# Performance work log

Hardware: AMD Instinct MI355X
Metric: run time of the kernel (lower is better)

Reference implementation:

```python
import jax, jax.numpy as jnp
import numpy as np

D_IN = 1024
D_OUT = 1024
SEQ = 2048
BATCH = 4


def setup_inputs() -> dict:
    key = jax.random.key(0)
    k_x, k_q, k_k, k_v = jax.random.split(key, 4)
    scale = 1.0 / np.sqrt(D_IN)  # ~ torch Linear init scale
    x = jax.random.normal(k_x, (BATCH, SEQ, D_IN), dtype=jnp.float32)
    # torch nn.Linear weights have shape [d_out, d_in]; y = x @ W.T
    Wq = jax.random.uniform(k_q, (D_OUT, D_IN), jnp.float32, -scale, scale)
    Wk = jax.random.uniform(k_k, (D_OUT, D_IN), jnp.float32, -scale, scale)
    Wv = jax.random.uniform(k_v, (D_OUT, D_IN), jnp.float32, -scale, scale)
    return {"x": x, "Wq": Wq, "Wk": Wk, "Wv": Wv}


def reference(x, Wq, Wk, Wv):
    # projections (no bias, qkv_bias=False)
    q = jnp.einsum("bsd,ed->bse", x, Wq)  # [B,S,D_OUT]
    k = jnp.einsum("bsd,ed->bse", x, Wk)
    v = jnp.einsum("bsd,ed->bse", x, Wv)
    scores = jnp.einsum("bqe,bke->bqk", q, k)  # [B,S,S]
    seq = scores.shape[-1]
    causal = jnp.tril(jnp.ones((seq, seq), dtype=bool))  # keep lower-tri
    scores = jnp.where(causal[None], scores, -jnp.inf)
    # note: original scales AFTER masking: softmax(scores / sqrt(d_k))
    inv_sqrt_dk = 1.0 / np.sqrt(k.shape[-1]).astype(np.float32)
    weights = jax.nn.softmax(scores * inv_sqrt_dk, axis=-1)
    # dropout p=0.0 (eval-equivalent): identity
    return jnp.einsum("bqk,bke->bqe", weights, v)
```

## Files before the change

kernel.cpp:

```cpp
#include <hip/hip_runtime.h>
#include <hip/hip_bf16.h>

typedef __bf16 v8bf __attribute__((ext_vector_type(8)));
typedef float v4f __attribute__((ext_vector_type(4)));

#define GBL_AS(p) ((const __attribute__((address_space(1))) unsigned int*)(p))
#define LDS_AS(p) ((__attribute__((address_space(3))) unsigned int*)(p))

#define WAIT_VM4() __builtin_amdgcn_s_waitcnt(0x0F74)
#define WAIT_VM6() __builtin_amdgcn_s_waitcnt(0x0F76)
#define WAIT_VM0() __builtin_amdgcn_s_waitcnt(0x0F70)

__global__ void cast_f32_bf16(const float* __restrict__ src,
                              __hip_bfloat16* __restrict__ dst, int n) {
  int i = (blockIdx.x * 256 + threadIdx.x) * 4;
  if (i >= n) return;
  float4 f = *(const float4*)(src + i);
  union { __hip_bfloat16 h[4]; uint2 u; } pk;
  pk.h[0] = __float2bfloat16(f.x);
  pk.h[1] = __float2bfloat16(f.y);
  pk.h[2] = __float2bfloat16(f.z);
  pk.h[3] = __float2bfloat16(f.w);
  *(uint2*)(dst + i) = pk.u;
}

__global__ void cast_w3(const float* __restrict__ a, const float* __restrict__ b,
                        const float* __restrict__ c, __hip_bfloat16* __restrict__ dst) {
  int seg = blockIdx.x >> 10;
  const float* src = seg == 0 ? a : (seg == 1 ? b : c);
  int i = ((blockIdx.x & 1023) * 256 + threadIdx.x) * 4;
  float4 f = *(const float4*)(src + i);
  union { __hip_bfloat16 h[4]; uint2 u; } pk;
  pk.h[0] = __float2bfloat16(f.x);
  pk.h[1] = __float2bfloat16(f.y);
  pk.h[2] = __float2bfloat16(f.z);
  pk.h[3] = __float2bfloat16(f.w);
  *(uint2*)(dst + seg * 1048576 + i) = pk.u;
}

__global__ __launch_bounds__(256, 2)
void gemm_proj(const __hip_bfloat16* __restrict__ A, int lda,
               const __hip_bfloat16* __restrict__ B, long sBb, int ldb,
               __hip_bfloat16* __restrict__ C, long sCb, int ldc,
               float scale, __hip_bfloat16* __restrict__ vTp) {
  const int tid = threadIdx.x;
  const int l = tid & 63, w = tid >> 6;
  const int z  = blockIdx.x >> 3;
  const int nb = (blockIdx.x & 7) << 7;
  const int mb = blockIdx.y << 8;

  B += (long)z * sBb;

  __shared__ alignas(16) __hip_bfloat16 As[3][256 * 32];
  __shared__ alignas(16) __hip_bfloat16 Bs[3][128 * 32];

  v4f acc[8][4] = {};
  const int wm = (w >> 1) << 7;
  const int wn = (w & 1) << 6;

  const int qa0 = 0 * 256 + w * 64 + l, ra0 = qa0 >> 2;
  const int qa1 = 1 * 256 + w * 64 + l, ra1 = qa1 >> 2;
  const int qa2 = 2 * 256 + w * 64 + l, ra2 = qa2 >> 2;
  const int qa3 = 3 * 256 + w * 64 + l, ra3 = qa3 >> 2;
  const __hip_bfloat16* sA0 = A + (long)(mb + ra0) * lda + (((qa0 & 3) ^ ((ra0 >> 1) & 3)) << 3);
  const __hip_bfloat16* sA1 = A + (long)(mb + ra1) * lda + (((qa1 & 3) ^ ((ra1 >> 1) & 3)) << 3);
  const __hip_bfloat16* sA2 = A + (long)(mb + ra2) * lda + (((qa2 & 3) ^ ((ra2 >> 1) & 3)) << 3);
  const __hip_bfloat16* sA3 = A + (long)(mb + ra3) * lda + (((qa3 & 3) ^ ((ra3 >> 1) & 3)) << 3);
  const int qb0 = 0 * 256 + w * 64 + l, rb0 = qb0 >> 2;
  const int qb1 = 1 * 256 + w * 64 + l, rb1 = qb1 >> 2;
  const __hip_bfloat16* sB0 = B + (long)(nb + rb0) * ldb + (((qb0 & 3) ^ ((rb0 >> 1) & 3)) << 3);
  const __hip_bfloat16* sB1 = B + (long)(nb + rb1) * ldb + (((qb1 & 3) ^ ((rb1 >> 1) & 3)) << 3);

  const int arow = wm + (l & 15);
  const int ldsA = arow * 32 + ((((l >> 4) ^ ((arow >> 1) & 3))) << 3);
  const int brow = wn + (l & 15);
  const int ldsB = brow * 32 + ((((l >> 4) ^ ((brow >> 1) & 3))) << 3);

#define STAGE_P(K0, BUF) do {                                                   \
    __builtin_amdgcn_global_load_lds(GBL_AS(sA0 + (K0)),                        \
        LDS_AS(&As[BUF][0 * 2048 + w * 512]), 16, 0, 0);                        \
    __builtin_amdgcn_global_load_lds(GBL_AS(sA1 + (K0)),                        \
        LDS_AS(&As[BUF][1 * 2048 + w * 512]), 16, 0, 0);                        \
    __builtin_amdgcn_global_load_lds(GBL_AS(sA2 + (K0)),                        \
        LDS_AS(&As[BUF][2 * 2048 + w * 512]), 16, 0, 0);                        \
    __builtin_amdgcn_global_load_lds(GBL_AS(sA3 + (K0)),                        \
        LDS_AS(&As[BUF][3 * 2048 + w * 512]), 16, 0, 0);                        \
    __builtin_amdgcn_global_load_lds(GBL_AS(sB0 + (K0)),                        \
        LDS_AS(&Bs[BUF][0 * 2048 + w * 512]), 16, 0, 0);                        \
    __builtin_amdgcn_global_load_lds(GBL_AS(sB1 + (K0)),                        \
        LDS_AS(&Bs[BUF][1 * 2048 + w * 512]), 16, 0, 0);                        \
  } while (0)

#define COMPUTE_P(BI) do {                                                      \
    v8bf af[8], bfr[4];                                                         \
    _Pragma("unroll")                                                           \
    for (int i = 0; i < 8; ++i)                                                 \
      af[i]  = *(const v8bf*)(&As[BI][ldsA + i * 512]);                         \
    _Pragma("unroll")                                                           \
    for (int j = 0; j < 4; ++j)                                                 \
      bfr[j] = *(const v8bf*)(&Bs[BI][ldsB + j * 512]);                         \
    _Pragma("unroll")                                                           \
    for (int i = 0; i < 8; ++i)                                                 \
      _Pragma("unroll")                                                         \
      for (int j = 0; j < 4; ++j)                                               \
        acc[i][j] = __builtin_amdgcn_mfma_f32_16x16x32_bf16(af[i], bfr[j],      \
                                                            acc[i][j], 0, 0, 0);\
  } while (0)

#define KITER_P(IT) do {                                                        \
    if constexpr ((IT) < 31) WAIT_VM6(); else WAIT_VM0();                       \
    __builtin_amdgcn_s_barrier();                                               \
    if constexpr ((IT) < 30) STAGE_P((IT) * 32 + 64, ((IT) + 2) % 3);           \
    COMPUTE_P((IT) % 3);                                                        \
  } while (0)

  STAGE_P(0, 0);
  STAGE_P(32, 1);
  KITER_P(0);  KITER_P(1);  KITER_P(2);  KITER_P(3);  KITER_P(4);  KITER_P(5);
  KITER_P(6);  KITER_P(7);  KITER_P(8);  KITER_P(9);  KITER_P(10); KITER_P(11);
  KITER_P(12); KITER_P(13); KITER_P(14); KITER_P(15); KITER_P(16); KITER_P(17);
  KITER_P(18); KITER_P(19); KITER_P(20); KITER_P(21); KITER_P(22); KITER_P(23);
  KITER_P(24); KITER_P(25); KITER_P(26); KITER_P(27); KITER_P(28); KITER_P(29);
  KITER_P(30); KITER_P(31);
#undef KITER_P
#undef COMPUTE_P
#undef STAGE_P

  const int col0 = nb + wn + (l & 15);
  const int row0 = mb + wm + ((l >> 4) << 2);
  if (z < 2) {
    __hip_bfloat16* Cz = C + (long)z * sCb;
#pragma unroll
    for (int i = 0; i < 8; ++i)
#pragma unroll
      for (int r = 0; r < 4; ++r) {
        long ro = (long)(row0 + i * 16 + r) * ldc;
#pragma unroll
        for (int j = 0; j < 4; ++j)
          Cz[ro + col0 + j * 16] = __float2bfloat16(acc[i][j][r] * scale);
      }
  } else {
    const long b = row0 >> 11;
    const int seq0 = row0 & 2047;
#pragma unroll
    for (int i = 0; i < 8; ++i)
#pragma unroll
      for (int j = 0; j < 4; ++j) {
        union { __hip_bfloat16 h[4]; uint2 u; } pk;
#pragma unroll
        for (int r = 0; r < 4; ++r) pk.h[r] = __float2bfloat16(acc[i][j][r]);
        *(uint2*)(vTp + b * 2097152 + (long)(col0 + j * 16) * 2048 +
                  (seq0 + i * 16)) = pk.u;
      }
  }
}

__global__ __launch_bounds__(256, 3)
void gemm_score(const __hip_bfloat16* __restrict__ A, long sAb,
                const __hip_bfloat16* __restrict__ B, long sBb,
                __hip_bfloat16* __restrict__ C, long sCb,
                float scale, float* __restrict__ sums) {
  const int tid = threadIdx.x;
  const int l = tid & 63, w = tid >> 6;
  const int id = blockIdx.x;
  const int wk = (id & 7) * 68 + (id >> 3);
  const int z = wk / 136;
  const int t = wk - z * 136;
  int m = (int)((__builtin_sqrtf(8.0f * t + 1.0f) - 1.0f) * 0.5f);
  while ((m + 1) * (m + 2) / 2 <= t) ++m;
  while (m * (m + 1) / 2 > t) --m;
  const int mb = m << 7;
  const int nb = (t - m * (m + 1) / 2) << 7;

  const __hip_bfloat16* Az = A + (long)z * sAb;
  const __hip_bfloat16* Bz = B + (long)z * sBb;

  __shared__ alignas(16) __hip_bfloat16 As[3][128 * 32];
  __shared__ alignas(16) __hip_bfloat16 Bs[3][128 * 32];

  v4f acc[4][4] = {};
  const int wm = (w >> 1) * 64, wn = (w & 1) * 64;

  const int cb0 = w * 64;
  const int q0 = cb0 + l, r0s = q0 >> 2;
  const int c0s = ((q0 & 3) ^ ((r0s >> 1) & 3)) << 3;
  const int cb1 = 256 + w * 64;
  const int q1 = cb1 + l, r1s = q1 >> 2;
  const int c1s = ((q1 & 3) ^ ((r1s >> 1) & 3)) << 3;

  const __hip_bfloat16* Arow0 = Az + (long)(mb + r0s) * 1024 + c0s;
  const __hip_bfloat16* Arow1 = Az + (long)(mb + r1s) * 1024 + c1s;
  const __hip_bfloat16* Brow0 = Bz + (long)(nb + r0s) * 1024 + c0s;
  const __hip_bfloat16* Brow1 = Bz + (long)(nb + r1s) * 1024 + c1s;

  const int arow = wm + (l & 15);
  const int ldsA = arow * 32 + ((((l >> 4) ^ ((arow >> 1) & 3))) << 3);
  const int brow = wn + (l & 15);
  const int ldsB = brow * 32 + ((((l >> 4) ^ ((brow >> 1) & 3))) << 3);

#define STAGE_S(K0, BUF) do {                                                   \
    __builtin_amdgcn_global_load_lds(GBL_AS(Arow0 + (K0)),                      \
        LDS_AS(&As[BUF][cb0 * 8]), 16, 0, 0);                                   \
    __builtin_amdgcn_global_load_lds(GBL_AS(Brow0 + (K0)),                      \
        LDS_AS(&Bs[BUF][cb0 * 8]), 16, 0, 0);                                   \
    __builtin_amdgcn_global_load_lds(GBL_AS(Arow1 + (K0)),                      \
        LDS_AS(&As[BUF][cb1 * 8]), 16, 0, 0);                                   \
    __builtin_amdgcn_global_load_lds(GBL_AS(Brow1 + (K0)),                      \
        LDS_AS(&Bs[BUF][cb1 * 8]), 16, 0, 0);                                   \
  } while (0)

#define COMPUTE_S(BI) do {                                                      \
    v8bf af[4], bfr[4];                                                         \
    _Pragma("unroll")                                                           \
    for (int i = 0; i < 4; ++i) {                                               \
      af[i]  = *(const v8bf*)(&As[BI][ldsA + i * 512]);                         \
      bfr[i] = *(const v8bf*)(&Bs[BI][ldsB + i * 512]);                         \
    }                                                                           \
    _Pragma("unroll")                                                           \
    for (int i = 0; i < 4; ++i)                                                 \
      _Pragma("unroll")                                                         \
      for (int j = 0; j < 4; ++j)                                               \
        acc[i][j] = __builtin_amdgcn_mfma_f32_16x16x32_bf16(af[i], bfr[j],      \
                                                            acc[i][j], 0, 0, 0);\
  } while (0)

#define KITER_S(IT) do {                                                        \
    if constexpr ((IT) < 31) WAIT_VM4(); else WAIT_VM0();                       \
    __builtin_amdgcn_s_barrier();                                               \
    if constexpr ((IT) < 30) STAGE_S((IT) * 32 + 64, ((IT) + 2) % 3);           \
    COMPUTE_S((IT) % 3);                                                        \
  } while (0)

  STAGE_S(0, 0);
  STAGE_S(32, 1);
  KITER_S(0);  KITER_S(1);  KITER_S(2);  KITER_S(3);  KITER_S(4);  KITER_S(5);
  KITER_S(6);  KITER_S(7);  KITER_S(8);  KITER_S(9);  KITER_S(10); KITER_S(11);
  KITER_S(12); KITER_S(13); KITER_S(14); KITER_S(15); KITER_S(16); KITER_S(17);
  KITER_S(18); KITER_S(19); KITER_S(20); KITER_S(21); KITER_S(22); KITER_S(23);
  KITER_S(24); KITER_S(25); KITER_S(26); KITER_S(27); KITER_S(28); KITER_S(29);
  KITER_S(30); KITER_S(31);
#undef KITER_S
#undef COMPUTE_S
#undef STAGE_S

  __hip_bfloat16* Cz = C + (long)z * sCb;
  float* srow = sums + z * 2048;
  const int col0 = nb + wn + (l & 15);
  const int row0 = mb + wm + ((l >> 4) << 2);
#pragma unroll
  for (int i = 0; i < 4; ++i)
#pragma unroll
    for (int r = 0; r < 4; ++r) {
      const int mm = row0 + i * 16 + r;
      const long ro = (long)mm * 2048;
      float sp = 0.f;
#pragma unroll
      for (int j = 0; j < 4; ++j) {
        const int n = col0 + j * 16;
        float pv = (n <= mm) ? __expf(acc[i][j][r] * scale) : 0.0f;
        sp += pv;
        Cz[ro + n] = __float2bfloat16(pv);
      }
      sp += __shfl_xor(sp, 1);
      sp += __shfl_xor(sp, 2);
      sp += __shfl_xor(sp, 4);
      sp += __shfl_xor(sp, 8);
      if ((l & 15) == 0) atomicAdd(&srow[mm], sp);
    }
}

__global__ __launch_bounds__(256, 3)
void gemm_pv(const __hip_bfloat16* __restrict__ A, long sAb, int lda,
             const __hip_bfloat16* __restrict__ B, long sBb, int ldb,
             float* __restrict__ C, long sCb, int ldc,
             const float* __restrict__ sums) {
  const int tid = threadIdx.x;
  const int l = tid & 63, w = tid >> 6;
  const int id = blockIdx.x;
  const int x = id & 7, j = id >> 3;
  const int z = x >> 1;
  const int nb = (((x & 1) << 2) | (j & 3)) << 7;
  const int m = 15 - (j >> 2);
  const int mb = m << 7;
  const int kend = (m + 1) << 7;

  A += (long)z * sAb;
  B += (long)z * sBb;

  __shared__ alignas(16) __hip_bfloat16 As[3][128 * 32];
  __shared__ alignas(16) __hip_bfloat16 Bs[3][128 * 32];

  v4f acc[4][4] = {};
  const int wm = (w >> 1) * 64, wn = (w & 1) * 64;

  const int cb0 = w * 64;
  const int q0 = cb0 + l, r0s = q0 >> 2;
  const int c0s = ((q0 & 3) ^ ((r0s >> 1) & 3)) << 3;
  const int cb1 = 256 + w * 64;
  const int q1 = cb1 + l, r1s = q1 >> 2;
  const int c1s = ((q1 & 3) ^ ((r1s >> 1) & 3)) << 3;

  const __hip_bfloat16* Arow0 = A + (long)(mb + r0s) * lda + c0s;
  const __hip_bfloat16* Arow1 = A + (long)(mb + r1s) * lda + c1s;
  const __hip_bfloat16* Brow0 = B + (long)(nb + r0s) * ldb + c0s;
  const __hip_bfloat16* Brow1 = B + (long)(nb + r1s) * ldb + c1s;

  const int arow = wm + (l & 15);
  const int ldsA = arow * 32 + ((((l >> 4) ^ ((arow >> 1) & 3))) << 3);
  const int brow = wn + (l & 15);
  const int ldsB = brow * 32 + ((((l >> 4) ^ ((brow >> 1) & 3))) << 3);

  auto stage = [&](int k0, int buf) {
    __builtin_amdgcn_global_load_lds(GBL_AS(Arow0 + k0),
        LDS_AS(&As[buf][cb0 * 8]), 16, 0, 0);
    __builtin_amdgcn_global_load_lds(GBL_AS(Brow0 + k0),
        LDS_AS(&Bs[buf][cb0 * 8]), 16, 0, 0);
    __builtin_amdgcn_global_load_lds(GBL_AS(Arow1 + k0),
        LDS_AS(&As[buf][cb1 * 8]), 16, 0, 0);
    __builtin_amdgcn_global_load_lds(GBL_AS(Brow1 + k0),
        LDS_AS(&Bs[buf][cb1 * 8]), 16, 0, 0);
  };
  stage(0, 0);
  if (32 < kend) stage(32, 1);
  int bi = 0;
  for (int k0 = 0; k0 < kend; k0 += 32) {
    if (k0 + 32 < kend) WAIT_VM4(); else WAIT_VM0();
    __builtin_amdgcn_s_barrier();
    if (k0 + 64 < kend) stage(k0 + 64, bi == 0 ? 2 : bi - 1);
    v8bf af[4], bfr[4];
#pragma unroll
    for (int i = 0; i < 4; ++i) {
      af[i]  = *(const v8bf*)(&As[bi][ldsA + i * 512]);
      bfr[i] = *(const v8bf*)(&Bs[bi][ldsB + i * 512]);
    }
#pragma unroll
    for (int i = 0; i < 4; ++i)
#pragma unroll
      for (int jj = 0; jj < 4; ++jj)
        acc[i][jj] = __builtin_amdgcn_mfma_f32_16x16x32_bf16(af[i], bfr[jj], acc[i][jj], 0, 0, 0);
    bi = (bi == 2) ? 0 : bi + 1;
  }

  float* Cz = C + (long)z * sCb;
  const float* srow = sums + z * 2048;
  const int col0 = nb + wn + (l & 15);
  const int row0 = mb + wm + ((l >> 4) << 2);
#pragma unroll
  for (int i = 0; i < 4; ++i)
#pragma unroll
    for (int r = 0; r < 4; ++r) {
      const int mr = row0 + i * 16 + r;
      const float sc = 1.0f / srow[mr];
      const long ro = (long)mr * ldc;
#pragma unroll
      for (int jj = 0; jj < 4; ++jj)
        Cz[ro + col0 + jj * 16] = acc[i][jj][r] * sc;
    }
}

extern "C" void kernel_launch(void* const* d_in, const int* in_sizes, int n_in,
                              void* d_out, int out_size, void* d_ws, size_t ws_size,
                              hipStream_t stream) {
  const float* x  = (const float*)d_in[0];
  const float* Wq = (const float*)d_in[1];
  const float* Wk = (const float*)d_in[2];
  const float* Wv = (const float*)d_in[3];
  float* out = (float*)d_out;
  char* ws = (char*)d_ws;

  __hip_bfloat16* qkv = (__hip_bfloat16*)ws;
  __hip_bfloat16* vT  = (__hip_bfloat16*)(ws + 50331648);
  __hip_bfloat16* xb  = (__hip_bfloat16*)(ws + 67108864);
  __hip_bfloat16* Wb  = (__hip_bfloat16*)(ws + 83886080);
  __hip_bfloat16* P   = (__hip_bfloat16*)(ws + 67108864);
  float* sums         = (float*)(ws + 100663296);

  hipMemsetAsync(sums, 0, 8192 * sizeof(float), stream);

  cast_f32_bf16<<<8192, 256, 0, stream>>>(x, xb, 8388608);
  cast_w3<<<3072, 256, 0, stream>>>(Wq, Wk, Wv, Wb);

  gemm_proj<<<dim3(24, 32, 1), 256, 0, stream>>>(
      xb, 1024, Wb, 1048576L, 1024, qkv, 8388608L, 1024, 1.0f, vT);

  gemm_score<<<dim3(544, 1, 1), 256, 0, stream>>>(
      qkv, 2097152L, qkv + 8388608, 2097152L,
      P, 4194304L, 0.03125f, sums);

  gemm_pv<<<dim3(512, 1, 1), 256, 0, stream>>>(
      P, 4194304L, 2048, vT, 2097152L, 2048,
      out, 2097152L, 1024, sums);
}
```

Measured before the change: 230.8 us.

## Enlarge score and PV GEMM tiles to 256x128 with per-wave 128x64 outputs

Both the causal score GEMM and the P·V GEMM now use 256x128 block tiles, with each wave computing a 128x64 sub-tile (8x4 MFMA accumulators) instead of 128x128 tiles with 64x64 per wave. The score kernel's triangular tile enumeration is reworked for 256-row blocks, and both grids shrink (544→288 and 512→256 blocks), with launch bounds lowered to 2 blocks per CU. The aim is more MFMA work per LDS fragment load and less global traffic per FLOP. The cost is higher register and LDS use, lower occupancy, fewer blocks to spread over the CUs, and extra masked work on the diagonal.

```diff
diff --git a/kernel.cpp b/kernel.cpp
--- a/kernel.cpp
+++ b/kernel.cpp
@@ -7,7 +7,6 @@
 #define GBL_AS(p) ((const __attribute__((address_space(1))) unsigned int*)(p))
 #define LDS_AS(p) ((__attribute__((address_space(3))) unsigned int*)(p))
 
-#define WAIT_VM4() __builtin_amdgcn_s_waitcnt(0x0F74)
 #define WAIT_VM6() __builtin_amdgcn_s_waitcnt(0x0F76)
 #define WAIT_VM0() __builtin_amdgcn_s_waitcnt(0x0F70)
 
@@ -37,6 +36,7 @@
   pk.h[3] = __float2bfloat16(f.w);
   *(uint2*)(dst + seg * 1048576 + i) = pk.u;
 }
+
 
 __global__ __launch_bounds__(256, 2)
 void gemm_proj(const __hip_bfloat16* __restrict__ A, int lda,
@@ -155,7 +155,7 @@
   }
 }
 
-__global__ __launch_bounds__(256, 3)
+__global__ __launch_bounds__(256, 2)
 void gemm_score(const __hip_bfloat16* __restrict__ A, long sAb,
                 const __hip_bfloat16* __restrict__ B, long sBb,
                 __hip_bfloat16* __restrict__ C, long sCb,
@@ -163,101 +163,108 @@
   const int tid = threadIdx.x;
   const int l = tid & 63, w = tid >> 6;
   const int id = blockIdx.x;
-  const int wk = (id & 7) * 68 + (id >> 3);
-  const int z = wk / 136;
-  const int t = wk - z * 136;
-  int m = (int)((__builtin_sqrtf(8.0f * t + 1.0f) - 1.0f) * 0.5f);
-  while ((m + 1) * (m + 2) / 2 <= t) ++m;
-  while (m * (m + 1) / 2 > t) --m;
-  const int mb = m << 7;
-  const int nb = (t - m * (m + 1) / 2) << 7;
+  const int wk = (id & 7) * 36 + (id >> 3);
+  const int z = wk / 72;
+  const int t = wk - z * 72;
+  int m2 = (int)(__builtin_sqrtf((float)t));
+  while ((m2 + 1) * (m2 + 2) <= t) ++m2;
+  while (m2 * (m2 + 1) > t) --m2;
+  const int mb = m2 << 8;
+  const int nb = (t - m2 * (m2 + 1)) << 7;
 
   const __hip_bfloat16* Az = A + (long)z * sAb;
   const __hip_bfloat16* Bz = B + (long)z * sBb;
 
-  __shared__ alignas(16) __hip_bfloat16 As[3][128 * 32];
+  __shared__ alignas(16) __hip_bfloat16 As[3][256 * 32];
   __shared__ alignas(16) __hip_bfloat16 Bs[3][128 * 32];
 
-  v4f acc[4][4] = {};
-  const int wm = (w >> 1) * 64, wn = (w & 1) * 64;
-
-  const int cb0 = w * 64;
-  const int q0 = cb0 + l, r0s = q0 >> 2;
-  const int c0s = ((q0 & 3) ^ ((r0s >> 1) & 3)) << 3;
-  const int cb1 = 256 + w * 64;
-  const int q1 = cb1 + l, r1s = q1 >> 2;
-  const int c1s = ((q1 & 3) ^ ((r1s >> 1) & 3)) << 3;
-
-  const __hip_bfloat16* Arow0 = Az + (long)(mb + r0s) * 1024 + c0s;
-  const __hip_bfloat16* Arow1 = Az + (long)(mb + r1s) * 1024 + c1s;
-  const __hip_bfloat16* Brow0 = Bz + (long)(nb + r0s) * 1024 + c0s;
-  const __hip_bfloat16* Brow1 = Bz + (long)(nb + r1s) * 1024 + c1s;
+  v4f acc[8][4] = {};
+  const int wm = (w >> 1) << 7;
+  const int wn = (w & 1) << 6;
+
+  const int qa0 = 0 * 256 + w * 64 + l, ra0 = qa0 >> 2;
+  const int qa1 = 1 * 256 + w * 64 + l, ra1 = qa1 >> 2;
+  const int qa2 = 2 * 256 + w * 64 + l, ra2 = qa2 >> 2;
+  const int qa3 = 3 * 256 + w * 64 + l, ra3 = qa3 >> 2;
+  const __hip_bfloat16* sA0 = Az + (long)(mb + ra0) * 1024 + (((qa0 & 3) ^ ((ra0 >> 1) & 3)) << 3);
+  const __hip_bfloat16* sA1 = Az + (long)(mb + ra1) * 1024 + (((qa1 & 3) ^ ((ra1 >> 1) & 3)) << 3);
+  const __hip_bfloat16* sA2 = Az + (long)(mb + ra2) * 1024 + (((qa2 & 3) ^ ((ra2 >> 1) & 3)) << 3);
+  const __hip_bfloat16* sA3 = Az + (long)(mb + ra3) * 1024 + (((qa3 & 3) ^ ((ra3 >> 1) & 3)) << 3);
+  const int qb0 = 0 * 256 + w * 64 + l, rb0 = qb0 >> 2;
+  const int qb1 = 1 * 256 + w * 64 + l, rb1 = qb1 >> 2;
+  const __hip_bfloat16* sB0 = Bz + (long)(nb + rb0) * 1024 + (((qb0 & 3) ^ ((rb0 >> 1) & 3)) << 3);
+  const __hip_bfloat16* sB1 = Bz + (long)(nb + rb1) * 1024 + (((qb1 & 3) ^ ((rb1 >> 1) & 3)) << 3);
 
   const int arow = wm + (l & 15);
   const int ldsA = arow * 32 + ((((l >> 4) ^ ((arow >> 1) & 3))) << 3);
   const int brow = wn + (l & 15);
   const int ldsB = brow * 32 + ((((l >> 4) ^ ((brow >> 1) & 3))) << 3);
 
-#define STAGE_S(K0, BUF) do {                                                   \
-    __builtin_amdgcn_global_load_lds(GBL_AS(Arow0 + (K0)),                      \
-        LDS_AS(&As[BUF][cb0 * 8]), 16, 0, 0);                                   \
-    __builtin_amdgcn_global_load_lds(GBL_AS(Brow0 + (K0)),                      \
-        LDS_AS(&Bs[BUF][cb0 * 8]), 16, 0, 0);                                   \
-    __builtin_amdgcn_global_load_lds(GBL_AS(Arow1 + (K0)),                      \
-        LDS_AS(&As[BUF][cb1 * 8]), 16, 0, 0);                                   \
-    __builtin_amdgcn_global_load_lds(GBL_AS(Brow1 + (K0)),                      \
-        LDS_AS(&Bs[BUF][cb1 * 8]), 16, 0, 0);                                   \
-  } while (0)
-
-#define COMPUTE_S(BI) do {                                                      \
-    v8bf af[4], bfr[4];                                                         \
-    _Pragma("unroll")                                                           \
-    for (int i = 0; i < 4; ++i) {                                               \
+#define STAGE_Q(K0, BUF) do {                                                   \
+    __builtin_amdgcn_global_load_lds(GBL_AS(sA0 + (K0)),                        \
+        LDS_AS(&As[BUF][0 * 2048 + w * 512]), 16, 0, 0);                        \
+    __builtin_amdgcn_global_load_lds(GBL_AS(sA1 + (K0)),                        \
+        LDS_AS(&As[BUF][1 * 2048 + w * 512]), 16, 0, 0);                        \
+    __builtin_amdgcn_global_load_lds(GBL_AS(sA2 + (K0)),                        \
+        LDS_AS(&As[BUF][2 * 2048 + w * 512]), 16, 0, 0);                        \
+    __builtin_amdgcn_global_load_lds(GBL_AS(sA3 + (K0)),                        \
+        LDS_AS(&As[BUF][3 * 2048 + w * 512]), 16, 0, 0);                        \
+    __builtin_amdgcn_global_load_lds(GBL_AS(sB0 + (K0)),                        \
+        LDS_AS(&Bs[BUF][0 * 2048 + w * 512]), 16, 0, 0);                        \
+    __builtin_amdgcn_global_load_lds(GBL_AS(sB1 + (K0)),                        \
+        LDS_AS(&Bs[BUF][1 * 2048 + w * 512]), 16, 0, 0);                        \
+  } while (0)
+
+#define COMPUTE_Q(BI) do {                                                      \
+    v8bf af[8], bfr[4];                                                         \
+    _Pragma("unroll")                                                           \
+    for (int i = 0; i < 8; ++i)                                                 \
       af[i]  = *(const v8bf*)(&As[BI][ldsA + i * 512]);                         \
-      bfr[i] = *(const v8bf*)(&Bs[BI][ldsB + i * 512]);                         \
-    }                                                                           \
-    _Pragma("unroll")                                                           \
-    for (int i = 0; i < 4; ++i)                                                 \
+    _Pragma("unroll")                                                           \
+    for (int j = 0; j < 4; ++j)                                                 \
+      bfr[j] = *(const v8bf*)(&Bs[BI][ldsB + j * 512]);                         \
+    _Pragma("unroll")                                                           \
+    for (int i = 0; i < 8; ++i)                                                 \
       _Pragma("unroll")                                                         \
       for (int j = 0; j < 4; ++j)                                               \
         acc[i][j] = __builtin_amdgcn_mfma_f32_16x16x32_bf16(af[i], bfr[j],      \
                                                             acc[i][j], 0, 0, 0);\
   } while (0)
 
-#define KITER_S(IT) do {                                                        \
-    if constexpr ((IT) < 31) WAIT_VM4(); else WAIT_VM0();                       \
+#define KITER_Q(IT) do {                                                        \
+    if constexpr ((IT) < 31) WAIT_VM6(); else WAIT_VM0();                       \
     __builtin_amdgcn_s_barrier();                                               \
-    if constexpr ((IT) < 30) STAGE_S((IT) * 32 + 64, ((IT) + 2) % 3);           \
-    COMPUTE_S((IT) % 3);                                                        \
-  } while (0)
-
-  STAGE_S(0, 0);
-  STAGE_S(32, 1);
-  KITER_S(0);  KITER_S(1);  KITER_S(2);  KITER_S(3);  KITER_S(4);  KITER_S(5);
-  KITER_S(6);  KITER_S(7);  KITER_S(8);  KITER_S(9);  KITER_S(10); KITER_S(11);
-  KITER_S(12); KITER_S(13); KITER_S(14); KITER_S(15); KITER_S(16); KITER_S(17);
-  KITER_S(18); KITER_S(19); KITER_S(20); KITER_S(21); KITER_S(22); KITER_S(23);
-  KITER_S(24); KITER_S(25); KITER_S(26); KITER_S(27); KITER_S(28); KITER_S(29);
-  KITER_S(30); KITER_S(31);
-#undef KITER_S
-#undef COMPUTE_S
-#undef STAGE_S
+    if constexpr ((IT) < 30) STAGE_Q((IT) * 32 + 64, ((IT) + 2) % 3);           \
+    COMPUTE_Q((IT) % 3);                                                        \
+  } while (0)
+
+  STAGE_Q(0, 0);
+  STAGE_Q(32, 1);
+  KITER_Q(0);  KITER_Q(1);  KITER_Q(2);  KITER_Q(3);  KITER_Q(4);  KITER_Q(5);
+  KITER_Q(6);  KITER_Q(7);  KITER_Q(8);  KITER_Q(9);  KITER_Q(10); KITER_Q(11);
+  KITER_Q(12); KITER_Q(13); KITER_Q(14); KITER_Q(15); KITER_Q(16); KITER_Q(17);
+  KITER_Q(18); KITER_Q(19); KITER_Q(20); KITER_Q(21); KITER_Q(22); KITER_Q(23);
+  KITER_Q(24); KITER_Q(25); KITER_Q(26); KITER_Q(27); KITER_Q(28); KITER_Q(29);
+  KITER_Q(30); KITER_Q(31);
+#undef KITER_Q
+#undef COMPUTE_Q
+#undef STAGE_Q
 
   __hip_bfloat16* Cz = C + (long)z * sCb;
   float* srow = sums + z * 2048;
   const int col0 = nb + wn + (l & 15);
   const int row0 = mb + wm + ((l >> 4) << 2);
 #pragma unroll
-  for (int i = 0; i < 4; ++i)
+  for (int i = 0; i < 8; ++i)
 #pragma unroll
     for (int r = 0; r < 4; ++r) {
-      const int mm = row0 + i * 16 + r;
-      const long ro = (long)mm * 2048;
+      const int m = row0 + i * 16 + r;
+      const long ro = (long)m * 2048;
       float sp = 0.f;
 #pragma unroll
       for (int j = 0; j < 4; ++j) {
         const int n = col0 + j * 16;
-        float pv = (n <= mm) ? __expf(acc[i][j][r] * scale) : 0.0f;
+        float pv = (n <= m) ? __expf(acc[i][j][r] * scale) : 0.0f;
         sp += pv;
         Cz[ro + n] = __float2bfloat16(pv);
       }
@@ -265,11 +272,11 @@
       sp += __shfl_xor(sp, 2);
       sp += __shfl_xor(sp, 4);
       sp += __shfl_xor(sp, 8);
-      if ((l & 15) == 0) atomicAdd(&srow[mm], sp);
+      if ((l & 15) == 0) atomicAdd(&srow[m], sp);
     }
 }
 
-__global__ __launch_bounds__(256, 3)
+__global__ __launch_bounds__(256, 2)
 void gemm_pv(const __hip_bfloat16* __restrict__ A, long sAb, int lda,
              const __hip_bfloat16* __restrict__ B, long sBb, int ldb,
              float* __restrict__ C, long sCb, int ldc,
@@ -277,33 +284,35 @@
   const int tid = threadIdx.x;
   const int l = tid & 63, w = tid >> 6;
   const int id = blockIdx.x;
-  const int x = id & 7, j = id >> 3;
-  const int z = x >> 1;
-  const int nb = (((x & 1) << 2) | (j & 3)) << 7;
-  const int m = 15 - (j >> 2);
-  const int mb = m << 7;
-  const int kend = (m + 1) << 7;
+  const int wk = (id & 7) * 32 + (id >> 3);
+  const int z = wk >> 6;
+  const int r6 = wk & 63;
+  const int m2 = r6 >> 3, c = r6 & 7;
+  const int mb = m2 << 8, nb = c << 7;
+  const int kend = (m2 + 1) << 8;
 
   A += (long)z * sAb;
   B += (long)z * sBb;
 
-  __shared__ alignas(16) __hip_bfloat16 As[3][128 * 32];
+  __shared__ alignas(16) __hip_bfloat16 As[3][256 * 32];
   __shared__ alignas(16) __hip_bfloat16 Bs[3][128 * 32];
 
-  v4f acc[4][4] = {};
-  const int wm = (w >> 1) * 64, wn = (w & 1) * 64;
-
-  const int cb0 = w * 64;
-  const int q0 = cb0 + l, r0s = q0 >> 2;
-  const int c0s = ((q0 & 3) ^ ((r0s >> 1) & 3)) << 3;
-  const int cb1 = 256 + w * 64;
-  const int q1 = cb1 + l, r1s = q1 >> 2;
-  const int c1s = ((q1 & 3) ^ ((r1s >> 1) & 3)) << 3;
-
-  const __hip_bfloat16* Arow0 = A + (long)(mb + r0s) * lda + c0s;
-  const __hip_bfloat16* Arow1 = A + (long)(mb + r1s) * lda + c1s;
-  const __hip_bfloat16* Brow0 = B + (long)(nb + r0s) * ldb + c0s;
-  const __hip_bfloat16* Brow1 = B + (long)(nb + r1s) * ldb + c1s;
+  v4f acc[8][4] = {};
+  const int wm = (w >> 1) << 7;
+  const int wn = (w & 1) << 6;
+
+  const int qa0 = 0 * 256 + w * 64 + l, ra0 = qa0 >> 2;
+  const int qa1 = 1 * 256 + w * 64 + l, ra1 = qa1 >> 2;
+  const int qa2 = 2 * 256 + w * 64 + l, ra2 = qa2 >> 2;
+  const int qa3 = 3 * 256 + w * 64 + l, ra3 = qa3 >> 2;
+  const __hip_bfloat16* sA0 = A + (long)(mb + ra0) * lda + (((qa0 & 3) ^ ((ra0 >> 1) & 3)) << 3);
+  const __hip_bfloat16* sA1 = A + (long)(mb + ra1) * lda + (((qa1 & 3) ^ ((ra1 >> 1) & 3)) << 3);
+  const __hip_bfloat16* sA2 = A + (long)(mb + ra2) * lda + (((qa2 & 3) ^ ((ra2 >> 1) & 3)) << 3);
+  const __hip_bfloat16* sA3 = A + (long)(mb + ra3) * lda + (((qa3 & 3) ^ ((ra3 >> 1) & 3)) << 3);
+  const int qb0 = 0 * 256 + w * 64 + l, rb0 = qb0 >> 2;
+  const int qb1 = 1 * 256 + w * 64 + l, rb1 = qb1 >> 2;
+  const __hip_bfloat16* sB0 = B + (long)(nb + rb0) * ldb + (((qb0 & 3) ^ ((rb0 >> 1) & 3)) << 3);
+  const __hip_bfloat16* sB1 = B + (long)(nb + rb1) * ldb + (((qb1 & 3) ^ ((rb1 >> 1) & 3)) << 3);
 
   const int arow = wm + (l & 15);
   const int ldsA = arow * 32 + ((((l >> 4) ^ ((arow >> 1) & 3))) << 3);
@@ -311,33 +320,38 @@
   const int ldsB = brow * 32 + ((((l >> 4) ^ ((brow >> 1) & 3))) << 3);
 
   auto stage = [&](int k0, int buf) {
-    __builtin_amdgcn_global_load_lds(GBL_AS(Arow0 + k0),
-        LDS_AS(&As[buf][cb0 * 8]), 16, 0, 0);
-    __builtin_amdgcn_global_load_lds(GBL_AS(Brow0 + k0),
-        LDS_AS(&Bs[buf][cb0 * 8]), 16, 0, 0);
-    __builtin_amdgcn_global_load_lds(GBL_AS(Arow1 + k0),
-        LDS_AS(&As[buf][cb1 * 8]), 16, 0, 0);
-    __builtin_amdgcn_global_load_lds(GBL_AS(Brow1 + k0),
-        LDS_AS(&Bs[buf][cb1 * 8]), 16, 0, 0);
+    __builtin_amdgcn_global_load_lds(GBL_AS(sA0 + k0),
+        LDS_AS(&As[buf][0 * 2048 + w * 512]), 16, 0, 0);
+    __builtin_amdgcn_global_load_lds(GBL_AS(sA1 + k0),
+        LDS_AS(&As[buf][1 * 2048 + w * 512]), 16, 0, 0);
+    __builtin_amdgcn_global_load_lds(GBL_AS(sA2 + k0),
+        LDS_AS(&As[buf][2 * 2048 + w * 512]), 16, 0, 0);
+    __builtin_amdgcn_global_load_lds(GBL_AS(sA3 + k0),
+        LDS_AS(&As[buf][3 * 2048 + w * 512]), 16, 0, 0);
+    __builtin_amdgcn_global_load_lds(GBL_AS(sB0 + k0),
+        LDS_AS(&Bs[buf][0 * 2048 + w * 512]), 16, 0, 0);
+    __builtin_amdgcn_global_load_lds(GBL_AS(sB1 + k0),
+        LDS_AS(&Bs[buf][1 * 2048 + w * 512]), 16, 0, 0);
   };
   stage(0, 0);
   if (32 < kend) stage(32, 1);
   int bi = 0;
   for (int k0 = 0; k0 < kend; k0 += 32) {
-    if (k0 + 32 < kend) WAIT_VM4(); else WAIT_VM0();
+    if (k0 + 32 < kend) WAIT_VM6(); else WAIT_VM0();
     __builtin_amdgcn_s_barrier();
     if (k0 + 64 < kend) stage(k0 + 64, bi == 0 ? 2 : bi - 1);
-    v8bf af[4], bfr[4];
-#pragma unroll
-    for (int i = 0; i < 4; ++i) {
+    v8bf af[8], bfr[4];
+#pragma unroll
+    for (int i = 0; i < 8; ++i)
       af[i]  = *(const v8bf*)(&As[bi][ldsA + i * 512]);
-      bfr[i] = *(const v8bf*)(&Bs[bi][ldsB + i * 512]);
-    }
-#pragma unroll
-    for (int i = 0; i < 4; ++i)
-#pragma unroll
-      for (int jj = 0; jj < 4; ++jj)
-        acc[i][jj] = __builtin_amdgcn_mfma_f32_16x16x32_bf16(af[i], bfr[jj], acc[i][jj], 0, 0, 0);
+#pragma unroll
+    for (int j = 0; j < 4; ++j)
+      bfr[j] = *(const v8bf*)(&Bs[bi][ldsB + j * 512]);
+#pragma unroll
+    for (int i = 0; i < 8; ++i)
+#pragma unroll
+      for (int j = 0; j < 4; ++j)
+        acc[i][j] = __builtin_amdgcn_mfma_f32_16x16x32_bf16(af[i], bfr[j], acc[i][j], 0, 0, 0);
     bi = (bi == 2) ? 0 : bi + 1;
   }
 
@@ -346,15 +360,15 @@
   const int col0 = nb + wn + (l & 15);
   const int row0 = mb + wm + ((l >> 4) << 2);
 #pragma unroll
-  for (int i = 0; i < 4; ++i)
+  for (int i = 0; i < 8; ++i)
 #pragma unroll
     for (int r = 0; r < 4; ++r) {
       const int mr = row0 + i * 16 + r;
       const float sc = 1.0f / srow[mr];
       const long ro = (long)mr * ldc;
 #pragma unroll
-      for (int jj = 0; jj < 4; ++jj)
-        Cz[ro + col0 + jj * 16] = acc[i][jj][r] * sc;
+      for (int j = 0; j < 4; ++j)
+        Cz[ro + col0 + j * 16] = acc[i][j][r] * sc;
     }
 }
 
@@ -383,11 +397,11 @@
   gemm_proj<<<dim3(24, 32, 1), 256, 0, stream>>>(
       xb, 1024, Wb, 1048576L, 1024, qkv, 8388608L, 1024, 1.0f, vT);
 
-  gemm_score<<<dim3(544, 1, 1), 256, 0, stream>>>(
+  gemm_score<<<dim3(288, 1, 1), 256, 0, stream>>>(
       qkv, 2097152L, qkv + 8388608, 2097152L,
       P, 4194304L, 0.03125f, sums);
 
-  gemm_pv<<<dim3(512, 1, 1), 256, 0, stream>>>(
+  gemm_pv<<<dim3(256, 1, 1), 256, 0, stream>>>(
       P, 4194304L, 2048, vT, 2097152L, 2048,
       out, 2097152L, 1024, sums);
 }
```

New measurement: 258.5 us. 1.12x slower.

## Fuse score and PV GEMMs into persistent ticket-scheduled kernel with row-block dependencies

Applied to the files above, without the earlier changes.

Replaces the separate score and PV kernel launches with one persistent kernel. Each block takes work items from an atomic ticket counter: the first 544 tickets compute causal score tiles and signal per-(batch,row-block) done counters, and the remaining tickets run PV tiles after spinning until their row block is complete. The aim is to overlap the PV stage with the tail of the score stage and remove the gap between the two launches. The cost is spin-wait latency, the atomics, and reliance on forward progress under the ticket order, which is safe because producers always hold lower tickets than consumers.

```diff
diff --git a/kernel.cpp b/kernel.cpp
--- a/kernel.cpp
+++ b/kernel.cpp
@@ -156,47 +156,57 @@
 }
 
 __global__ __launch_bounds__(256, 3)
-void gemm_score(const __hip_bfloat16* __restrict__ A, long sAb,
-                const __hip_bfloat16* __restrict__ B, long sBb,
-                __hip_bfloat16* __restrict__ C, long sCb,
-                float scale, float* __restrict__ sums) {
+void attn_sp(const __hip_bfloat16* __restrict__ q,
+             const __hip_bfloat16* __restrict__ kk,
+             __hip_bfloat16* __restrict__ P,
+             const __hip_bfloat16* __restrict__ vT,
+             float* __restrict__ out,
+             float* __restrict__ sums,
+             int* __restrict__ ticket,
+             int* __restrict__ done) {
   const int tid = threadIdx.x;
   const int l = tid & 63, w = tid >> 6;
-  const int id = blockIdx.x;
-  const int wk = (id & 7) * 68 + (id >> 3);
-  const int z = wk / 136;
-  const int t = wk - z * 136;
-  int m = (int)((__builtin_sqrtf(8.0f * t + 1.0f) - 1.0f) * 0.5f);
-  while ((m + 1) * (m + 2) / 2 <= t) ++m;
-  while (m * (m + 1) / 2 > t) --m;
-  const int mb = m << 7;
-  const int nb = (t - m * (m + 1) / 2) << 7;
-
-  const __hip_bfloat16* Az = A + (long)z * sAb;
-  const __hip_bfloat16* Bz = B + (long)z * sBb;
 
   __shared__ alignas(16) __hip_bfloat16 As[3][128 * 32];
   __shared__ alignas(16) __hip_bfloat16 Bs[3][128 * 32];
-
-  v4f acc[4][4] = {};
+  __shared__ int s_t;
+
   const int wm = (w >> 1) * 64, wn = (w & 1) * 64;
-
   const int cb0 = w * 64;
-  const int q0 = cb0 + l, r0s = q0 >> 2;
-  const int c0s = ((q0 & 3) ^ ((r0s >> 1) & 3)) << 3;
+  const int q0i = cb0 + l, r0s = q0i >> 2;
+  const int c0s = ((q0i & 3) ^ ((r0s >> 1) & 3)) << 3;
   const int cb1 = 256 + w * 64;
-  const int q1 = cb1 + l, r1s = q1 >> 2;
-  const int c1s = ((q1 & 3) ^ ((r1s >> 1) & 3)) << 3;
-
-  const __hip_bfloat16* Arow0 = Az + (long)(mb + r0s) * 1024 + c0s;
-  const __hip_bfloat16* Arow1 = Az + (long)(mb + r1s) * 1024 + c1s;
-  const __hip_bfloat16* Brow0 = Bz + (long)(nb + r0s) * 1024 + c0s;
-  const __hip_bfloat16* Brow1 = Bz + (long)(nb + r1s) * 1024 + c1s;
-
+  const int q1i = cb1 + l, r1s = q1i >> 2;
+  const int c1s = ((q1i & 3) ^ ((r1s >> 1) & 3)) << 3;
   const int arow = wm + (l & 15);
   const int ldsA = arow * 32 + ((((l >> 4) ^ ((arow >> 1) & 3))) << 3);
   const int brow = wn + (l & 15);
   const int ldsB = brow * 32 + ((((l >> 4) ^ ((brow >> 1) & 3))) << 3);
+
+  for (;;) {
+    __syncthreads();
+    if (tid == 0) s_t = atomicAdd(ticket, 1);
+    __syncthreads();
+    const int t = s_t;
+    if (t >= 1056) return;
+
+    if (t < 544) {
+      int m = (int)((__builtin_sqrtf(2.0f * t + 1.0f) - 1.0f) * 0.5f);
+      while (2 * (m + 1) * (m + 2) <= t) ++m;
+      while (2 * m * (m + 1) > t) --m;
+      const int rem = t - 2 * m * (m + 1);
+      const int z = rem / (m + 1);
+      const int n = rem - z * (m + 1);
+      const int mb = m << 7, nb = n << 7;
+
+      const __hip_bfloat16* Az = q  + (long)z * 2097152;
+      const __hip_bfloat16* Bz = kk + (long)z * 2097152;
+      const __hip_bfloat16* Arow0 = Az + (long)(mb + r0s) * 1024 + c0s;
+      const __hip_bfloat16* Arow1 = Az + (long)(mb + r1s) * 1024 + c1s;
+      const __hip_bfloat16* Brow0 = Bz + (long)(nb + r0s) * 1024 + c0s;
+      const __hip_bfloat16* Brow1 = Bz + (long)(nb + r1s) * 1024 + c1s;
+
+      v4f acc[4][4] = {};
 
 #define STAGE_S(K0, BUF) do {                                                   \
     __builtin_amdgcn_global_load_lds(GBL_AS(Arow0 + (K0)),                      \
@@ -231,131 +241,126 @@
     COMPUTE_S((IT) % 3);                                                        \
   } while (0)
 
-  STAGE_S(0, 0);
-  STAGE_S(32, 1);
-  KITER_S(0);  KITER_S(1);  KITER_S(2);  KITER_S(3);  KITER_S(4);  KITER_S(5);
-  KITER_S(6);  KITER_S(7);  KITER_S(8);  KITER_S(9);  KITER_S(10); KITER_S(11);
-  KITER_S(12); KITER_S(13); KITER_S(14); KITER_S(15); KITER_S(16); KITER_S(17);
-  KITER_S(18); KITER_S(19); KITER_S(20); KITER_S(21); KITER_S(22); KITER_S(23);
-  KITER_S(24); KITER_S(25); KITER_S(26); KITER_S(27); KITER_S(28); KITER_S(29);
-  KITER_S(30); KITER_S(31);
+      STAGE_S(0, 0);
+      STAGE_S(32, 1);
+      KITER_S(0);  KITER_S(1);  KITER_S(2);  KITER_S(3);  KITER_S(4);
+      KITER_S(5);  KITER_S(6);  KITER_S(7);  KITER_S(8);  KITER_S(9);
+      KITER_S(10); KITER_S(11); KITER_S(12); KITER_S(13); KITER_S(14);
+      KITER_S(15); KITER_S(16); KITER_S(17); KITER_S(18); KITER_S(19);
+      KITER_S(20); KITER_S(21); KITER_S(22); KITER_S(23); KITER_S(24);
+      KITER_S(25); KITER_S(26); KITER_S(27); KITER_S(28); KITER_S(29);
+      KITER_S(30); KITER_S(31);
 #undef KITER_S
 #undef COMPUTE_S
 #undef STAGE_S
 
-  __hip_bfloat16* Cz = C + (long)z * sCb;
-  float* srow = sums + z * 2048;
-  const int col0 = nb + wn + (l & 15);
-  const int row0 = mb + wm + ((l >> 4) << 2);
-#pragma unroll
-  for (int i = 0; i < 4; ++i)
-#pragma unroll
-    for (int r = 0; r < 4; ++r) {
-      const int mm = row0 + i * 16 + r;
-      const long ro = (long)mm * 2048;
-      float sp = 0.f;
-#pragma unroll
-      for (int j = 0; j < 4; ++j) {
-        const int n = col0 + j * 16;
-        float pv = (n <= mm) ? __expf(acc[i][j][r] * scale) : 0.0f;
-        sp += pv;
-        Cz[ro + n] = __float2bfloat16(pv);
-      }
-      sp += __shfl_xor(sp, 1);
-      sp += __shfl_xor(sp, 2);
-      sp += __shfl_xor(sp, 4);
-      sp += __shfl_xor(sp, 8);
-      if ((l & 15) == 0) atomicAdd(&srow[mm], sp);
+      __hip_bfloat16* Cz = P + (long)z * 4194304;
+      float* srow = sums + z * 2048;
+      const int col0 = nb + wn + (l & 15);
+      const int row0 = mb + wm + ((l >> 4) << 2);
+#pragma unroll
+      for (int i = 0; i < 4; ++i)
+#pragma unroll
+        for (int r = 0; r < 4; ++r) {
+          const int mm = row0 + i * 16 + r;
+          const long ro = (long)mm * 2048;
+          float sp = 0.f;
+#pragma unroll
+          for (int j = 0; j < 4; ++j) {
+            const int nn = col0 + j * 16;
+            float pv = (nn <= mm) ? __expf(acc[i][j][r] * 0.03125f) : 0.0f;
+            sp += pv;
+            Cz[ro + nn] = __float2bfloat16(pv);
+          }
+          sp += __shfl_xor(sp, 1);
+          sp += __shfl_xor(sp, 2);
+          sp += __shfl_xor(sp, 4);
+          sp += __shfl_xor(sp, 8);
+          if ((l & 15) == 0) atomicAdd(&srow[mm], sp);
+        }
+
+      __threadfence();
+      __syncthreads();
+      if (tid == 0)
+        __hip_atomic_fetch_add(&done[z * 16 + m], 1,
+                               __ATOMIC_RELEASE, __HIP_MEMORY_SCOPE_AGENT);
+    } else {
+      const int u = t - 544;
+      const int m = u >> 5;
+      const int rem = u & 31;
+      const int z = rem >> 3, nc = rem & 7;
+      const int mb = m << 7, nb = nc << 7;
+      const int kend = (m + 1) << 7;
+
+      if (tid == 0) {
+        while (__hip_atomic_load(&done[z * 16 + m],
+                                 __ATOMIC_ACQUIRE, __HIP_MEMORY_SCOPE_AGENT) < m + 1)
+          __builtin_amdgcn_s_sleep(16);
+      }
+      __syncthreads();
+      {
+        int d = __hip_atomic_load(&done[z * 16 + m],
+                                  __ATOMIC_ACQUIRE, __HIP_MEMORY_SCOPE_AGENT);
+        asm volatile("" : : "v"(d));
+      }
+
+      const __hip_bfloat16* Az = P  + (long)z * 4194304;
+      const __hip_bfloat16* Bz = vT + (long)z * 2097152;
+      const __hip_bfloat16* Arow0 = Az + (long)(mb + r0s) * 2048 + c0s;
+      const __hip_bfloat16* Arow1 = Az + (long)(mb + r1s) * 2048 + c1s;
+      const __hip_bfloat16* Brow0 = Bz + (long)(nb + r0s) * 2048 + c0s;
+      const __hip_bfloat16* Brow1 = Bz + (long)(nb + r1s) * 2048 + c1s;
+
+      v4f acc[4][4] = {};
+      auto stage = [&](int k0, int buf) {
+        __builtin_amdgcn_global_load_lds(GBL_AS(Arow0 + k0),
+            LDS_AS(&As[buf][cb0 * 8]), 16, 0, 0);
+        __builtin_amdgcn_global_load_lds(GBL_AS(Brow0 + k0),
+            LDS_AS(&Bs[buf][cb0 * 8]), 16, 0, 0);
+        __builtin_amdgcn_global_load_lds(GBL_AS(Arow1 + k0),
+            LDS_AS(&As[buf][cb1 * 8]), 16, 0, 0);
+        __builtin_amdgcn_global_load_lds(GBL_AS(Brow1 + k0),
+            LDS_AS(&Bs[buf][cb1 * 8]), 16, 0, 0);
+      };
+      stage(0, 0);
+      if (32 < kend) stage(32, 1);
+      int bi = 0;
+      for (int k0 = 0; k0 < kend; k0 += 32) {
+        if (k0 + 32 < kend) WAIT_VM4(); else WAIT_VM0();
+        __builtin_amdgcn_s_barrier();
+        if (k0 + 64 < kend) stage(k0 + 64, bi == 0 ? 2 : bi - 1);
+        v8bf af[4], bfr[4];
+#pragma unroll
+        for (int i = 0; i < 4; ++i) {
+          af[i]  = *(const v8bf*)(&As[bi][ldsA + i * 512]);
+          bfr[i] = *(const v8bf*)(&Bs[bi][ldsB + i * 512]);
+        }
+#pragma unroll
+        for (int i = 0; i < 4; ++i)
+#pragma unroll
+          for (int jj = 0; jj < 4; ++jj)
+            acc[i][jj] = __builtin_amdgcn_mfma_f32_16x16x32_bf16(af[i], bfr[jj],
+                                                                 acc[i][jj], 0, 0, 0);
+        bi = (bi == 2) ? 0 : bi + 1;
+      }
+
+      float* Cz = out + (long)z * 2097152;
+      const float* srow = sums + z * 2048;
+      const int col0 = nb + wn + (l & 15);
+      const int row0 = mb + wm + ((l >> 4) << 2);
+#pragma unroll
+      for (int i = 0; i < 4; ++i)
+#pragma unroll
+        for (int r = 0; r < 4; ++r) {
+          const int mr = row0 + i * 16 + r;
+          const float sc = 1.0f / srow[mr];
+          const long ro = (long)mr * 1024;
+#pragma unroll
+          for (int jj = 0; jj < 4; ++jj)
+            Cz[ro + col0 + jj * 16] = acc[i][jj][r] * sc;
+        }
     }
-}
-
-__global__ __launch_bounds__(256, 3)
-void gemm_pv(const __hip_bfloat16* __restrict__ A, long sAb, int lda,
-             const __hip_bfloat16* __restrict__ B, long sBb, int ldb,
-             float* __restrict__ C, long sCb, int ldc,
-             const float* __restrict__ sums) {
-  const int tid = threadIdx.x;
-  const int l = tid & 63, w = tid >> 6;
-  const int id = blockIdx.x;
-  const int x = id & 7, j = id >> 3;
-  const int z = x >> 1;
-  const int nb = (((x & 1) << 2) | (j & 3)) << 7;
-  const int m = 15 - (j >> 2);
-  const int mb = m << 7;
-  const int kend = (m + 1) << 7;
-
-  A += (long)z * sAb;
-  B += (long)z * sBb;
-
-  __shared__ alignas(16) __hip_bfloat16 As[3][128 * 32];
-  __shared__ alignas(16) __hip_bfloat16 Bs[3][128 * 32];
-
-  v4f acc[4][4] = {};
-  const int wm = (w >> 1) * 64, wn = (w & 1) * 64;
-
-  const int cb0 = w * 64;
-  const int q0 = cb0 + l, r0s = q0 >> 2;
-  const int c0s = ((q0 & 3) ^ ((r0s >> 1) & 3)) << 3;
-  const int cb1 = 256 + w * 64;
-  const int q1 = cb1 + l, r1s = q1 >> 2;
-  const int c1s = ((q1 & 3) ^ ((r1s >> 1) & 3)) << 3;
-
-  const __hip_bfloat16* Arow0 = A + (long)(mb + r0s) * lda + c0s;
-  const __hip_bfloat16* Arow1 = A + (long)(mb + r1s) * lda + c1s;
-  const __hip_bfloat16* Brow0 = B + (long)(nb + r0s) * ldb + c0s;
-  const __hip_bfloat16* Brow1 = B + (long)(nb + r1s) * ldb + c1s;
-
-  const int arow = wm + (l & 15);
-  const int ldsA = arow * 32 + ((((l >> 4) ^ ((arow >> 1) & 3))) << 3);
-  const int brow = wn + (l & 15);
-  const int ldsB = brow * 32 + ((((l >> 4) ^ ((brow >> 1) & 3))) << 3);
-
-  auto stage = [&](int k0, int buf) {
-    __builtin_amdgcn_global_load_lds(GBL_AS(Arow0 + k0),
-        LDS_AS(&As[buf][cb0 * 8]), 16, 0, 0);
-    __builtin_amdgcn_global_load_lds(GBL_AS(Brow0 + k0),
-        LDS_AS(&Bs[buf][cb0 * 8]), 16, 0, 0);
-    __builtin_amdgcn_global_load_lds(GBL_AS(Arow1 + k0),
-        LDS_AS(&As[buf][cb1 * 8]), 16, 0, 0);
-    __builtin_amdgcn_global_load_lds(GBL_AS(Brow1 + k0),
-        LDS_AS(&Bs[buf][cb1 * 8]), 16, 0, 0);
-  };
-  stage(0, 0);
-  if (32 < kend) stage(32, 1);
-  int bi = 0;
-  for (int k0 = 0; k0 < kend; k0 += 32) {
-    if (k0 + 32 < kend) WAIT_VM4(); else WAIT_VM0();
-    __builtin_amdgcn_s_barrier();
-    if (k0 + 64 < kend) stage(k0 + 64, bi == 0 ? 2 : bi - 1);
-    v8bf af[4], bfr[4];
-#pragma unroll
-    for (int i = 0; i < 4; ++i) {
-      af[i]  = *(const v8bf*)(&As[bi][ldsA + i * 512]);
-      bfr[i] = *(const v8bf*)(&Bs[bi][ldsB + i * 512]);
-    }
-#pragma unroll
-    for (int i = 0; i < 4; ++i)
-#pragma unroll
-      for (int jj = 0; jj < 4; ++jj)
-        acc[i][jj] = __builtin_amdgcn_mfma_f32_16x16x32_bf16(af[i], bfr[jj], acc[i][jj], 0, 0, 0);
-    bi = (bi == 2) ? 0 : bi + 1;
   }
-
-  float* Cz = C + (long)z * sCb;
-  const float* srow = sums + z * 2048;
-  const int col0 = nb + wn + (l & 15);
-  const int row0 = mb + wm + ((l >> 4) << 2);
-#pragma unroll
-  for (int i = 0; i < 4; ++i)
-#pragma unroll
-    for (int r = 0; r < 4; ++r) {
-      const int mr = row0 + i * 16 + r;
-      const float sc = 1.0f / srow[mr];
-      const long ro = (long)mr * ldc;
-#pragma unroll
-      for (int jj = 0; jj < 4; ++jj)
-        Cz[ro + col0 + jj * 16] = acc[i][jj][r] * sc;
-    }
 }
 
 extern "C" void kernel_launch(void* const* d_in, const int* in_sizes, int n_in,
@@ -374,8 +379,10 @@
   __hip_bfloat16* Wb  = (__hip_bfloat16*)(ws + 83886080);
   __hip_bfloat16* P   = (__hip_bfloat16*)(ws + 67108864);
   float* sums         = (float*)(ws + 100663296);
-
-  hipMemsetAsync(sums, 0, 8192 * sizeof(float), stream);
+  int* ticket         = (int*)(ws + 100696064);
+  int* done           = (int*)(ws + 100696128);
+
+  hipMemsetAsync(sums, 0, 33792, stream);
 
   cast_f32_bf16<<<8192, 256, 0, stream>>>(x, xb, 8388608);
   cast_w3<<<3072, 256, 0, stream>>>(Wq, Wk, Wv, Wb);
@@ -383,11 +390,6 @@
   gemm_proj<<<dim3(24, 32, 1), 256, 0, stream>>>(
       xb, 1024, Wb, 1048576L, 1024, qkv, 8388608L, 1024, 1.0f, vT);
 
-  gemm_score<<<dim3(544, 1, 1), 256, 0, stream>>>(
-      qkv, 2097152L, qkv + 8388608, 2097152L,
-      P, 4194304L, 0.03125f, sums);
-
-  gemm_pv<<<dim3(512, 1, 1), 256, 0, stream>>>(
-      P, 4194304L, 2048, vT, 2097152L, 2048,
-      out, 2097152L, 1024, sums);
-}
+  attn_sp<<<dim3(768, 1, 1), 256, 0, stream>>>(
+      qkv, qkv + 8388608, P, vT, out, sums, ticket, done);
+}
```

New measurement: 424.4 us. +83.9%, slower.
